# Optimization experiments

Hardware: AMD Instinct MI355X
Metric: run time of the kernel (lower is better)

The kernel has to match this reference:

```python
import jax, jax.numpy as jnp
import numpy as np

LATENT = 1024
ENC = 4096
B = 8192


def setup_inputs() -> dict:
    key = jax.random.key(0)
    k1, k2, k3, k4 = jax.random.split(key, 4)
    inp = jax.random.normal(k1, (B, LATENT), dtype=jnp.float32)
    enc = jax.random.normal(k2, (B, ENC), dtype=jnp.float32)
    # nn.Linear(ENC, LATENT): weight [LATENT, ENC], bias [LATENT]
    bound = 1.0 / np.sqrt(ENC)
    W = jax.random.uniform(k3, (LATENT, ENC), minval=-bound, maxval=bound, dtype=jnp.float32)
    b = jax.random.uniform(k4, (LATENT,), minval=-bound, maxval=bound, dtype=jnp.float32)
    return {"input": inp, "encoder_output": enc, "W": W, "b": b}


def reference(input, encoder_output, W, b):
    # vector = Linear(encoder_output)  -> [B, LATENT]
    v = jnp.einsum("be,de->bd", encoder_output, W) + b
    # Fused Householder-style reflection (math identical to bmm(vv^T, x)):
    # out = x - 2 * v * (v . x) / ||v||   (original divides by norm, not norm^2)
    dot = jnp.sum(v * input, axis=1, keepdims=True)          # [B, 1]
    norm = jnp.linalg.norm(v, axis=1, keepdims=True)         # [B, 1]
    output = input - 2.0 * v * dot / norm                    # [B, LATENT]
    log_det = jnp.zeros((input.shape[0], 1), dtype=input.dtype)
    return (output, log_det)
```

## Files before the change

kernel.cpp:

```cpp
#include <hip/hip_runtime.h>
#include <hip/hip_bf16.h>
#include <stdint.h>

#define M_DIM 8192
#define N_DIM 1024
#define K_DIM 4096

typedef __bf16 bf16x8 __attribute__((ext_vector_type(8)));
typedef float f32x4 __attribute__((ext_vector_type(4)));
typedef __hip_bfloat16 bf16_t;

__device__ __forceinline__ void gload_lds16(const void* g, void* l) {
  __builtin_amdgcn_global_load_lds(
      (const __attribute__((address_space(1))) void*)g,
      (__attribute__((address_space(3))) void*)l, 16, 0, 0);
}

__global__ __launch_bounds__(256) void pack_both(const float* __restrict__ enc,
                                                 const float* __restrict__ W,
                                                 int4* __restrict__ pA,
                                                 int4* __restrict__ pB) {
  const unsigned gtid = blockIdx.x * 256 + threadIdx.x;
  const float* src;
  int4* dst;
  unsigned t;
  if (gtid < 4194304u) { src = enc; dst = pA; t = gtid; }
  else                 { src = W;   dst = pB; t = gtid - 4194304u; }
  const unsigned cp = t & 7;
  const unsigned tmp = t >> 3;
  const unsigned r = tmp & 255;
  const unsigned tmp2 = tmp >> 8;
  const unsigned kt = tmp2 & 63;
  const unsigned rt = tmp2 >> 6;
  const unsigned srow = (rt << 8) + r;
  const unsigned k0 = (kt << 6) + ((cp ^ (r & 7)) << 3);
  const float4* s = (const float4*)(src + (size_t)srow * 4096 + k0);
  float4 a = s[0], b = s[1];
  union { bf16_t h[8]; int4 v; } u;
  u.h[0] = __float2bfloat16(a.x); u.h[1] = __float2bfloat16(a.y);
  u.h[2] = __float2bfloat16(a.z); u.h[3] = __float2bfloat16(a.w);
  u.h[4] = __float2bfloat16(b.x); u.h[5] = __float2bfloat16(b.y);
  u.h[6] = __float2bfloat16(b.z); u.h[7] = __float2bfloat16(b.w);
  dst[t] = u.v;
}

__device__ __forceinline__ void stage_half(const char* g, char* smem, int ldsoff, int tid) {
  gload_lds16(g + tid * 16, smem + ldsoff + tid * 16);
  gload_lds16(g + 8192 + tid * 16, smem + ldsoff + 8192 + tid * 16);
}

__global__ __launch_bounds__(512, 2) void gemm8(
    const char* __restrict__ pA, const char* __restrict__ pB,
    float* __restrict__ V0, float* __restrict__ V1p, int NT) {
  extern __shared__ char smem[];
  const int tid = threadIdx.x;
  const int lane = tid & 63, wave = tid >> 6;
  const int wm = wave >> 2, wn = wave & 3;
  const int lrow = lane & 15, lkc = lane >> 4;

  const int cpx = (int)gridDim.x >> 3;
  const int swz = ((int)blockIdx.x & 7) * cpx + ((int)blockIdx.x >> 3);
  const int split = swz >> 7;
  const int rem = swz & 127;
  const int mt = rem >> 2, nt = rem & 3;

  const char* Abase = pA + ((size_t)mt * 64 + (size_t)split * NT) * 32768;
  const char* Bbase = pB + ((size_t)nt * 64 + (size_t)split * NT) * 32768;
  float* V = split ? V1p : V0;

  int colw[2];
  colw[0] = ((lkc) ^ (lrow & 7)) << 4;
  colw[1] = ((4 + lkc) ^ (lrow & 7)) << 4;
  int aRow[4], bRow[2];
  #pragma unroll
  for (int f = 0; f < 4; ++f) aRow[f] = (wm * 64 + f * 16 + lrow) * 128;
  #pragma unroll
  for (int f2 = 0; f2 < 2; ++f2) bRow[f2] = 32768 + (wn * 32 + f2 * 16 + lrow) * 128;

  f32x4 acc[2][4][2][2];
  #pragma unroll
  for (int a0 = 0; a0 < 2; ++a0)
    #pragma unroll
    for (int a1 = 0; a1 < 4; ++a1)
      #pragma unroll
      for (int a2 = 0; a2 < 2; ++a2)
        #pragma unroll
        for (int a3 = 0; a3 < 2; ++a3)
          acc[a0][a1][a2][a3] = (f32x4){0.f, 0.f, 0.f, 0.f};

  const int ktm = NT - 1;

  stage_half(Abase,         smem, 0, tid);
  stage_half(Abase + 16384, smem, 16384, tid);
  stage_half(Bbase,         smem, 32768, tid);
  stage_half(Bbase + 16384, smem, 49152, tid);
  stage_half(Abase + 32768, smem, 65536, tid);
  asm volatile("s_waitcnt vmcnt(2)" ::: "memory");
  __builtin_amdgcn_sched_barrier(0);
  __builtin_amdgcn_s_barrier();

  bf16x8 aE[4][2], aO[4][2], b0[2][2], b1[2][2];
  #pragma unroll
  for (int f = 0; f < 4; ++f)
    #pragma unroll
    for (int s = 0; s < 2; ++s)
      aE[f][s] = *(const bf16x8*)(smem + aRow[f] + colw[s]);
  #pragma unroll
  for (int f2 = 0; f2 < 2; ++f2)
    #pragma unroll
    for (int s = 0; s < 2; ++s)
      b0[f2][s] = *(const bf16x8*)(smem + bRow[f2] + colw[s]);

  for (int g = 0; g < NT; ++g) {
    const int bb = g & 1, nbf = bb ^ 1;
    char* ab = smem + bb * 65536;
    char* nb = smem + nbf * 65536;
    const char* A1t = Abase + (size_t)((g + 1) & ktm) * 32768;
    const char* B1t = Bbase + (size_t)((g + 1) & ktm) * 32768;
    const char* A2t = Abase + (size_t)((g + 2) & ktm) * 32768;

    #pragma unroll
    for (int f2 = 0; f2 < 2; ++f2)
      #pragma unroll
      for (int s = 0; s < 2; ++s)
        b1[f2][s] = *(const bf16x8*)(ab + bRow[f2] + 16384 + colw[s]);
    stage_half(B1t, smem, nbf * 65536 + 32768, tid);
    stage_half(A1t + 16384, smem, nbf * 65536 + 16384, tid);
    __builtin_amdgcn_s_setprio(1);
    #pragma unroll
    for (int f = 0; f < 4; ++f)
      #pragma unroll
      for (int f2 = 0; f2 < 2; ++f2)
        #pragma unroll
        for (int s = 0; s < 2; ++s)
          acc[0][f][0][f2] = __builtin_amdgcn_mfma_f32_16x16x32_bf16(
              aE[f][s], b0[f2][s], acc[0][f][0][f2], 0, 0, 0);
    __builtin_amdgcn_s_setprio(0);
    __builtin_amdgcn_sched_barrier(0);
    __builtin_amdgcn_s_barrier();

    #pragma unroll
    for (int f = 0; f < 4; ++f)
      #pragma unroll
      for (int s = 0; s < 2; ++s)
        aO[f][s] = *(const bf16x8*)(ab + aRow[f] + 16384 + colw[s]);
    __builtin_amdgcn_s_setprio(1);
    #pragma unroll
    for (int f = 0; f < 4; ++f)
      #pragma unroll
      for (int f2 = 0; f2 < 2; ++f2)
        #pragma unroll
        for (int s = 0; s < 2; ++s)
          acc[0][f][1][f2] = __builtin_amdgcn_mfma_f32_16x16x32_bf16(
              aE[f][s], b1[f2][s], acc[0][f][1][f2], 0, 0, 0);
    __builtin_amdgcn_s_setprio(0);
    asm volatile("s_waitcnt vmcnt(2)" ::: "memory");
    __builtin_amdgcn_sched_barrier(0);
    __builtin_amdgcn_s_barrier();

    #pragma unroll
    for (int f = 0; f < 4; ++f)
      #pragma unroll
      for (int s = 0; s < 2; ++s)
        aE[f][s] = *(const bf16x8*)(nb + aRow[f] + colw[s]);
    stage_half(B1t + 16384, smem, nbf * 65536 + 49152, tid);
    stage_half(A2t, smem, bb * 65536, tid);
    __builtin_amdgcn_s_setprio(1);
    #pragma unroll
    for (int f = 0; f < 4; ++f)
      #pragma unroll
      for (int f2 = 0; f2 < 2; ++f2)
        #pragma unroll
        for (int s = 0; s < 2; ++s)
          acc[1][f][1][f2] = __builtin_amdgcn_mfma_f32_16x16x32_bf16(
              aO[f][s], b1[f2][s], acc[1][f][1][f2], 0, 0, 0);
    __builtin_amdgcn_s_setprio(0);
    asm volatile("s_waitcnt vmcnt(4)" ::: "memory");
    __builtin_amdgcn_sched_barrier(0);
    __builtin_amdgcn_s_barrier();

    __builtin_amdgcn_s_setprio(1);
    #pragma unroll
    for (int f = 0; f < 4; ++f)
      #pragma unroll
      for (int f2 = 0; f2 < 2; ++f2)
        #pragma unroll
        for (int s = 0; s < 2; ++s)
          acc[1][f][0][f2] = __builtin_amdgcn_mfma_f32_16x16x32_bf16(
              aO[f][s], b0[f2][s], acc[1][f][0][f2], 0, 0, 0);
    __builtin_amdgcn_s_setprio(0);
    __builtin_amdgcn_sched_barrier(0);
    #pragma unroll
    for (int f2 = 0; f2 < 2; ++f2)
      #pragma unroll
      for (int s = 0; s < 2; ++s)
        b0[f2][s] = *(const bf16x8*)(nb + bRow[f2] + colw[s]);
    asm volatile("s_waitcnt vmcnt(2)" ::: "memory");
    __builtin_amdgcn_sched_barrier(0);
    __builtin_amdgcn_s_barrier();
  }

  const int lq = lane >> 4;
  #pragma unroll
  for (int qm = 0; qm < 2; ++qm)
    #pragma unroll
    for (int f = 0; f < 4; ++f) {
      const int rowg = mt * 256 + qm * 128 + wm * 64 + f * 16 + lq * 4;
      #pragma unroll
      for (int reg = 0; reg < 4; ++reg) {
        float* Vr = V + (size_t)(rowg + reg) * N_DIM + nt * 256 + wn * 32 + lrow;
        #pragma unroll
        for (int qn = 0; qn < 2; ++qn)
          #pragma unroll
          for (int f2 = 0; f2 < 2; ++f2)
            Vr[qn * 128 + f2 * 16] = acc[qm][f][qn][f2][reg];
      }
    }
}

__global__ __launch_bounds__(256) void householder_ep(
    const float* __restrict__ x, const float* __restrict__ bias,
    float* __restrict__ vio, const float* __restrict__ V2,
    float* __restrict__ logdet) {
  const int row = blockIdx.x;
  const int t = threadIdx.x;
  float4* vr = (float4*)(vio + (size_t)row * N_DIM);
  const float4* xr = (const float4*)(x + (size_t)row * N_DIM);
  const float4* br = (const float4*)bias;

  float4 v = vr[t];
  if (V2) {
    float4 v2 = ((const float4*)(V2 + (size_t)row * N_DIM))[t];
    v.x += v2.x; v.y += v2.y; v.z += v2.z; v.w += v2.w;
  }
  float4 bb = br[t];
  v.x += bb.x; v.y += bb.y; v.z += bb.z; v.w += bb.w;
  float4 xx = xr[t];

  float dot = v.x * xx.x + v.y * xx.y + v.z * xx.z + v.w * xx.w;
  float nsq = v.x * v.x + v.y * v.y + v.z * v.z + v.w * v.w;

  #pragma unroll
  for (int off = 32; off > 0; off >>= 1) {
    dot += __shfl_down(dot, off);
    nsq += __shfl_down(nsq, off);
  }
  __shared__ float sd[4], sn[4];
  if ((t & 63) == 0) { sd[t >> 6] = dot; sn[t >> 6] = nsq; }
  __syncthreads();
  dot = sd[0] + sd[1] + sd[2] + sd[3];
  nsq = sn[0] + sn[1] + sn[2] + sn[3];

  const float f = 2.0f * dot / sqrtf(nsq);
  float4 o;
  o.x = xx.x - f * v.x;
  o.y = xx.y - f * v.y;
  o.z = xx.z - f * v.z;
  o.w = xx.w - f * v.w;
  vr[t] = o;
  if (t == 0) logdet[row] = 0.0f;
}

extern "C" void kernel_launch(void* const* d_in, const int* in_sizes, int n_in,
                              void* d_out, int out_size, void* d_ws, size_t ws_size,
                              hipStream_t stream) {
  const float* x   = (const float*)d_in[0];
  const float* enc = (const float*)d_in[1];
  const float* W   = (const float*)d_in[2];
  const float* b   = (const float*)d_in[3];

  float* out    = (float*)d_out;
  float* v      = out;
  float* logdet = out + (size_t)M_DIM * N_DIM;

  char*  packA = (char*)d_ws;
  char*  packB = packA + (size_t)64 * 1024 * 1024;
  float* V2    = (float*)(packB + (size_t)8 * 1024 * 1024);

  const size_t need2 = (size_t)104 * 1024 * 1024;
  const int nsplit = (ws_size >= need2) ? 2 : 1;

  pack_both<<<18432, 256, 0, stream>>>(enc, W, (int4*)packA, (int4*)packB);

  hipFuncSetAttribute((const void*)gemm8, hipFuncAttributeMaxDynamicSharedMemorySize, 131072);
  gemm8<<<dim3(128 * nsplit), 512, 131072, stream>>>(
      packA, packB, v, nsplit == 2 ? V2 : nullptr, 64 / nsplit);

  householder_ep<<<M_DIM, 256, 0, stream>>>(x, b, v, nsplit == 2 ? V2 : nullptr, logdet);
}
```

Baseline: 119.5 us.

## Fuse fp32-to-bf16 conversion of encoder output into GEMM A-tile loading

Removes the separate pre-pass that packed the 128 MB fp32 encoder_output into a swizzled bf16 buffer. The GEMM now loads fp32 A rows directly into registers, converts them to bf16 and writes them into swizzled LDS, interleaved with the MFMA phases and with rescheduled waitcnts. This avoids writing and re-reading 64 MB of packed A and shrinks the workspace need. In exchange, A staging goes through VGPRs with extra VALU and LDS-write work inside the main loop, which may raise register pressure and cut overlap compared with direct global-to-LDS loads.

Result: slower. 180.2 us (+50.8%).

```diff
diff --git a/kernel.cpp b/kernel.cpp
--- a/kernel.cpp
+++ b/kernel.cpp
@@ -16,16 +16,9 @@
       (__attribute__((address_space(3))) void*)l, 16, 0, 0);
 }
 
-__global__ __launch_bounds__(256) void pack_both(const float* __restrict__ enc,
-                                                 const float* __restrict__ W,
-                                                 int4* __restrict__ pA,
-                                                 int4* __restrict__ pB) {
-  const unsigned gtid = blockIdx.x * 256 + threadIdx.x;
-  const float* src;
-  int4* dst;
-  unsigned t;
-  if (gtid < 4194304u) { src = enc; dst = pA; t = gtid; }
-  else                 { src = W;   dst = pB; t = gtid - 4194304u; }
+__global__ __launch_bounds__(256) void pack_w(const float* __restrict__ W,
+                                              int4* __restrict__ pB) {
+  const unsigned t = blockIdx.x * 256 + threadIdx.x;
   const unsigned cp = t & 7;
   const unsigned tmp = t >> 3;
   const unsigned r = tmp & 255;
@@ -34,14 +27,14 @@
   const unsigned rt = tmp2 >> 6;
   const unsigned srow = (rt << 8) + r;
   const unsigned k0 = (kt << 6) + ((cp ^ (r & 7)) << 3);
-  const float4* s = (const float4*)(src + (size_t)srow * 4096 + k0);
+  const float4* s = (const float4*)(W + (size_t)srow * 4096 + k0);
   float4 a = s[0], b = s[1];
   union { bf16_t h[8]; int4 v; } u;
   u.h[0] = __float2bfloat16(a.x); u.h[1] = __float2bfloat16(a.y);
   u.h[2] = __float2bfloat16(a.z); u.h[3] = __float2bfloat16(a.w);
   u.h[4] = __float2bfloat16(b.x); u.h[5] = __float2bfloat16(b.y);
   u.h[6] = __float2bfloat16(b.z); u.h[7] = __float2bfloat16(b.w);
-  dst[t] = u.v;
+  pB[t] = u.v;
 }
 
 __device__ __forceinline__ void stage_half(const char* g, char* smem, int ldsoff, int tid) {
@@ -49,8 +42,25 @@
   gload_lds16(g + 8192 + tid * 16, smem + ldsoff + 8192 + tid * 16);
 }
 
+__device__ __forceinline__ void issue4(const float* g, float4* r) {
+  r[0] = *(const float4*)(g);
+  r[1] = *(const float4*)(g + (size_t)32 * K_DIM);
+  r[2] = *(const float4*)(g + (size_t)64 * K_DIM);
+  r[3] = *(const float4*)(g + (size_t)96 * K_DIM);
+}
+
+__device__ __forceinline__ void cvt_write(const float4* r, char* base, int o0) {
+  #pragma unroll
+  for (int i = 0; i < 4; ++i) {
+    union { bf16_t h[4]; int2 v; } u;
+    u.h[0] = __float2bfloat16(r[i].x); u.h[1] = __float2bfloat16(r[i].y);
+    u.h[2] = __float2bfloat16(r[i].z); u.h[3] = __float2bfloat16(r[i].w);
+    *(int2*)(base + o0 + i * 4096) = u.v;
+  }
+}
+
 __global__ __launch_bounds__(512, 2) void gemm8(
-    const char* __restrict__ pA, const char* __restrict__ pB,
+    const float* __restrict__ Araw, const char* __restrict__ pB,
     float* __restrict__ V0, float* __restrict__ V1p, int NT) {
   extern __shared__ char smem[];
   const int tid = threadIdx.x;
@@ -64,9 +74,13 @@
   const int rem = swz & 127;
   const int mt = rem >> 2, nt = rem & 3;
 
-  const char* Abase = pA + ((size_t)mt * 64 + (size_t)split * NT) * 32768;
   const char* Bbase = pB + ((size_t)nt * 64 + (size_t)split * NT) * 32768;
   float* V = split ? V1p : V0;
+
+  const float* aG = Araw + (size_t)(mt * 256 + (tid >> 4)) * K_DIM +
+                    (size_t)split * (NT * 64) + (tid & 15) * 4;
+  const int wrO0 = (tid >> 4) * 128 + (((((tid & 15) >> 1)) ^ ((tid >> 4) & 7)) << 4) +
+                   ((tid & 15) & 1) * 8;
 
   int colw[2];
   colw[0] = ((lkc) ^ (lrow & 7)) << 4;
@@ -89,14 +103,22 @@
           acc[a0][a1][a2][a3] = (f32x4){0.f, 0.f, 0.f, 0.f};
 
   const int ktm = NT - 1;
-
-  stage_half(Abase,         smem, 0, tid);
-  stage_half(Abase + 16384, smem, 16384, tid);
-  stage_half(Bbase,         smem, 32768, tid);
+  float4 gab[4], gt[4];
+
+  issue4(aG, gab);
+  issue4(aG + (size_t)128 * K_DIM, gt);
+  stage_half(Bbase, smem, 32768, tid);
   stage_half(Bbase + 16384, smem, 49152, tid);
-  stage_half(Abase + 32768, smem, 65536, tid);
-  asm volatile("s_waitcnt vmcnt(2)" ::: "memory");
-  __builtin_amdgcn_sched_barrier(0);
+  asm volatile("s_waitcnt vmcnt(8)" ::: "memory");
+  cvt_write(gab, smem + 0, wrO0);
+  asm volatile("s_waitcnt vmcnt(4)" ::: "memory");
+  cvt_write(gt, smem + 16384, wrO0);
+  issue4(aG + 64, gab);
+  asm volatile("s_waitcnt vmcnt(4)" ::: "memory");
+  asm volatile("s_waitcnt vmcnt(0)" ::: "memory");
+  cvt_write(gab, smem + 65536, wrO0);
+  issue4(aG + 64 + (size_t)128 * K_DIM, gab);
+  asm volatile("s_waitcnt lgkmcnt(0)" ::: "memory");
   __builtin_amdgcn_s_barrier();
 
   bf16x8 aE[4][2], aO[4][2], b0[2][2], b1[2][2];
@@ -115,9 +137,8 @@
     const int bb = g & 1, nbf = bb ^ 1;
     char* ab = smem + bb * 65536;
     char* nb = smem + nbf * 65536;
-    const char* A1t = Abase + (size_t)((g + 1) & ktm) * 32768;
     const char* B1t = Bbase + (size_t)((g + 1) & ktm) * 32768;
-    const char* A2t = Abase + (size_t)((g + 2) & ktm) * 32768;
+    const size_t ka2 = (size_t)((g + 2) & ktm) * 64;
 
     #pragma unroll
     for (int f2 = 0; f2 < 2; ++f2)
@@ -125,7 +146,6 @@
       for (int s = 0; s < 2; ++s)
         b1[f2][s] = *(const bf16x8*)(ab + bRow[f2] + 16384 + colw[s]);
     stage_half(B1t, smem, nbf * 65536 + 32768, tid);
-    stage_half(A1t + 16384, smem, nbf * 65536 + 16384, tid);
     __builtin_amdgcn_s_setprio(1);
     #pragma unroll
     for (int f = 0; f < 4; ++f)
@@ -136,6 +156,10 @@
           acc[0][f][0][f2] = __builtin_amdgcn_mfma_f32_16x16x32_bf16(
               aE[f][s], b0[f2][s], acc[0][f][0][f2], 0, 0, 0);
     __builtin_amdgcn_s_setprio(0);
+    asm volatile("s_waitcnt vmcnt(2)" ::: "memory");
+    cvt_write(gab, nb + 16384, wrO0);
+    issue4(aG + ka2, gab);
+    asm volatile("s_waitcnt lgkmcnt(0)" ::: "memory");
     __builtin_amdgcn_sched_barrier(0);
     __builtin_amdgcn_s_barrier();
 
@@ -154,17 +178,10 @@
           acc[0][f][1][f2] = __builtin_amdgcn_mfma_f32_16x16x32_bf16(
               aE[f][s], b1[f2][s], acc[0][f][1][f2], 0, 0, 0);
     __builtin_amdgcn_s_setprio(0);
-    asm volatile("s_waitcnt vmcnt(2)" ::: "memory");
     __builtin_amdgcn_sched_barrier(0);
     __builtin_amdgcn_s_barrier();
 
-    #pragma unroll
-    for (int f = 0; f < 4; ++f)
-      #pragma unroll
-      for (int s = 0; s < 2; ++s)
-        aE[f][s] = *(const bf16x8*)(nb + aRow[f] + colw[s]);
     stage_half(B1t + 16384, smem, nbf * 65536 + 49152, tid);
-    stage_half(A2t, smem, bb * 65536, tid);
     __builtin_amdgcn_s_setprio(1);
     #pragma unroll
     for (int f = 0; f < 4; ++f)
@@ -175,10 +192,18 @@
           acc[1][f][1][f2] = __builtin_amdgcn_mfma_f32_16x16x32_bf16(
               aO[f][s], b1[f2][s], acc[1][f][1][f2], 0, 0, 0);
     __builtin_amdgcn_s_setprio(0);
-    asm volatile("s_waitcnt vmcnt(4)" ::: "memory");
+    asm volatile("s_waitcnt vmcnt(2)" ::: "memory");
+    cvt_write(gab, ab, wrO0);
+    issue4(aG + ka2 + (size_t)128 * K_DIM, gab);
+    asm volatile("s_waitcnt lgkmcnt(0)" ::: "memory");
     __builtin_amdgcn_sched_barrier(0);
     __builtin_amdgcn_s_barrier();
 
+    #pragma unroll
+    for (int f = 0; f < 4; ++f)
+      #pragma unroll
+      for (int s = 0; s < 2; ++s)
+        aE[f][s] = *(const bf16x8*)(nb + aRow[f] + colw[s]);
     __builtin_amdgcn_s_setprio(1);
     #pragma unroll
     for (int f = 0; f < 4; ++f)
@@ -195,7 +220,7 @@
       #pragma unroll
       for (int s = 0; s < 2; ++s)
         b0[f2][s] = *(const bf16x8*)(nb + bRow[f2] + colw[s]);
-    asm volatile("s_waitcnt vmcnt(2)" ::: "memory");
+    asm volatile("s_waitcnt vmcnt(4)" ::: "memory");
     __builtin_amdgcn_sched_barrier(0);
     __builtin_amdgcn_s_barrier();
   }
@@ -273,18 +298,17 @@
   float* v      = out;
   float* logdet = out + (size_t)M_DIM * N_DIM;
 
-  char*  packA = (char*)d_ws;
-  char*  packB = packA + (size_t)64 * 1024 * 1024;
+  char*  packB = (char*)d_ws;
   float* V2    = (float*)(packB + (size_t)8 * 1024 * 1024);
 
-  const size_t need2 = (size_t)104 * 1024 * 1024;
+  const size_t need2 = (size_t)40 * 1024 * 1024;
   const int nsplit = (ws_size >= need2) ? 2 : 1;
 
-  pack_both<<<18432, 256, 0, stream>>>(enc, W, (int4*)packA, (int4*)packB);
+  pack_w<<<2048, 256, 0, stream>>>(W, (int4*)packB);
 
   hipFuncSetAttribute((const void*)gemm8, hipFuncAttributeMaxDynamicSharedMemorySize, 131072);
   gemm8<<<dim3(128 * nsplit), 512, 131072, stream>>>(
-      packA, packB, v, nsplit == 2 ? V2 : nullptr, 64 / nsplit);
+      enc, packB, v, nsplit == 2 ? V2 : nullptr, 64 / nsplit);
 
   householder_ep<<<M_DIM, 256, 0, stream>>>(x, b, v, nsplit == 2 ? V2 : nullptr, logdet);
 }
```
